# Performance work log

Hardware: AMD Instinct MI355X
Metric: run time of the kernel (lower is better)

## Reference

```python
import jax, jax.numpy as jnp
import numpy as np

B, D_IN, D_H = 8192, 512, 1024


def setup_inputs() -> dict:
    key = jax.random.key(0)
    ks = jax.random.split(key, 5)
    # Kaiming-normal-ish init: std = sqrt(2/fan_in)
    Wx = jax.random.normal(ks[0], (D_IN, 4 * D_H), jnp.float32) * np.sqrt(2.0 / D_IN)
    Wh = jax.random.normal(ks[1], (D_H, 4 * D_H), jnp.float32) * np.sqrt(2.0 / D_H)
    b = jnp.zeros((4 * D_H,), jnp.float32)
    x = jax.random.normal(ks[2], (B, D_IN), jnp.float32)
    h = jax.random.normal(ks[3], (B, D_H), jnp.float32)
    c = jax.random.normal(ks[4], (B, D_H), jnp.float32)
    return {"x": x, "h": h, "c": c, "Wx": Wx, "Wh": Wh, "b": b}


def reference(x, h, c, Wx, Wh, b):
    # Fused gate pre-activations: [B, 4H] in gate order (g, i, f, o)
    gates = x @ Wx + h @ Wh + b[None, :]
    g_in, i_in, f_in, o_in = jnp.split(gates, 4, axis=-1)
    g_out = jnp.tanh(g_in)
    i_out = jax.nn.sigmoid(i_in)
    # NOTE: faithful to the original source's bug — f_out and o_out both use i_in.
    f_out = jax.nn.sigmoid(i_in)
    o_out = jax.nn.sigmoid(i_in)
    c_new = g_out * i_out + f_out * c
    h_new = jnp.tanh(c_new) * o_out
    return h_new, c_new
```

## Files before the change

### kernel.cpp

```cpp
#include <hip/hip_runtime.h>
#include <hip/hip_bf16.h>
#include <cstdint>

#define BROWS 8192
#define DIN   512
#define DH    1024
#define KTOT  1536
#define NT    (KTOT / 64)

typedef __bf16 bf16x8 __attribute__((ext_vector_type(8)));
typedef __bf16 bf16x4 __attribute__((ext_vector_type(4)));
typedef float  f32x4  __attribute__((ext_vector_type(4)));

__device__ __forceinline__ void load16_to_lds(const void* gptr, void* lptr) {
    __builtin_amdgcn_global_load_lds(
        (const __attribute__((address_space(1))) uint32_t*)gptr,
        (__attribute__((address_space(3))) uint32_t*)lptr,
        16, 0, 0);
}

__global__ __launch_bounds__(256) void cvtA_kernel(
    const float* __restrict__ x, const float* __restrict__ h,
    __bf16* __restrict__ A) {
    int t = blockIdx.x * 256 + threadIdx.x;
    int row = t / 192;
    int j = t - row * 192;
    int kg = j * 8;
    const float* src = (kg < DIN) ? (x + (size_t)row * DIN + kg)
                                  : (h + (size_t)row * DH + (kg - DIN));
    float4 u = *(const float4*)src;
    float4 v = *(const float4*)(src + 4);
    bf16x8 o = { (__bf16)u.x, (__bf16)u.y, (__bf16)u.z, (__bf16)u.w,
                 (__bf16)v.x, (__bf16)v.y, (__bf16)v.z, (__bf16)v.w };
    int swz = (j * 16) ^ ((row & 7) << 4);
    *(bf16x8*)((char*)A + (size_t)row * 3072 + swz) = o;
}

__global__ __launch_bounds__(256) void cvtB_kernel(
    const float* __restrict__ Wx, const float* __restrict__ Wh,
    __bf16* __restrict__ Bt) {
    __shared__ float tile[32][33];
    int k0 = blockIdx.x * 32;
    int n0 = blockIdx.y * 32;
    int tx = threadIdx.x;
    int ty = threadIdx.y;
#pragma unroll
    for (int i = 0; i < 4; ++i) {
        int k = k0 + ty + 8 * i;
        float v = (k < DIN) ? Wx[(size_t)k * 4096 + n0 + tx]
                            : Wh[(size_t)(k - DIN) * 4096 + n0 + tx];
        tile[ty + 8 * i][tx] = v;
    }
    __syncthreads();
    int n = n0 + tx;
    int kk = ty * 4;
    bf16x4 o = { (__bf16)tile[kk][tx], (__bf16)tile[kk + 1][tx],
                 (__bf16)tile[kk + 2][tx], (__bf16)tile[kk + 3][tx] };
    int swz = ((k0 + kk) * 2) ^ ((n & 7) << 4);
    *(bf16x4*)((char*)Bt + (size_t)n * 3072 + swz) = o;
}


#define BARRIER  do { __builtin_amdgcn_sched_barrier(0); __builtin_amdgcn_s_barrier(); __builtin_amdgcn_sched_barrier(0); } while (0)
#define VMW(n)   do { asm volatile("s_waitcnt vmcnt(" #n ")" ::: "memory"); __builtin_amdgcn_sched_barrier(0); } while (0)
#define LGKM0    do { asm volatile("s_waitcnt lgkmcnt(0)" ::: "memory"); __builtin_amdgcn_sched_barrier(0); } while (0)

#define STAGE_A(buf, kt) do {                                                  \
    _Pragma("unroll")                                                          \
    for (int p_ = 0; p_ < 4; ++p_) {                                           \
        int row_ = p_ * 32 + r0;                                               \
        load16_to_lds(Ab + (size_t)(brow + row_) * 3072 + (kt) * 128 + cb,     \
                      sAb + (buf) * 32768 + row_ * 128 + cb);                  \
    }                                                                          \
    __builtin_amdgcn_sched_barrier(0);                                         \
} while (0)

#define STAGE_BG(buf, kt) do {                                                 \
    _Pragma("unroll")                                                          \
    for (int p_ = 0; p_ < 2; ++p_) {                                           \
        int row_ = p_ * 32 + r0;                                               \
        load16_to_lds(Bb + (size_t)(bnp + row_) * 3072 + (kt) * 128 + cb,      \
                      sAb + (buf) * 32768 + 16384 + row_ * 128 + cb);          \
    }                                                                          \
    __builtin_amdgcn_sched_barrier(0);                                         \
} while (0)

#define STAGE_BI(buf, kt) do {                                                 \
    _Pragma("unroll")                                                          \
    for (int p_ = 0; p_ < 2; ++p_) {                                           \
        int row_ = p_ * 32 + r0;                                               \
        load16_to_lds(Bb + (size_t)(1024 + bnp + row_) * 3072                  \
                          + (kt) * 128 + cb,                                   \
                      sAb + (buf) * 32768 + 16384 + (64 + row_) * 128 + cb);   \
    }                                                                          \
    __builtin_amdgcn_sched_barrier(0);                                         \
} while (0)

#define READ_A(c)                                                              \
    _Pragma("unroll")                                                          \
    for (int m_ = 0; m_ < 4; ++m_) {                                           \
        _Pragma("unroll")                                                      \
        for (int ks_ = 0; ks_ < 2; ++ks_) {                                    \
            aF[m_][ks_] = *(const bf16x8*)(sAb + (c) * 32768                   \
                + (wrow + m_ * 16 + l15) * 128                                 \
                + ((ks_ * 64 + l4x16) ^ swzkey));                              \
        }                                                                      \
    }

#define READ_BG(c)                                                             \
    _Pragma("unroll")                                                          \
    for (int n_ = 0; n_ < 2; ++n_) {                                           \
        _Pragma("unroll")                                                      \
        for (int ks_ = 0; ks_ < 2; ++ks_) {                                    \
            bgF[n_][ks_] = *(const bf16x8*)(sAb + (c) * 32768 + 16384          \
                + (wcol + n_ * 16 + l15) * 128                                 \
                + ((ks_ * 64 + l4x16) ^ swzkey));                              \
        }                                                                      \
    }

#define READ_BI(c)                                                             \
    _Pragma("unroll")                                                          \
    for (int n_ = 0; n_ < 2; ++n_) {                                           \
        _Pragma("unroll")                                                      \
        for (int ks_ = 0; ks_ < 2; ++ks_) {                                    \
            biF[n_][ks_] = *(const bf16x8*)(sAb + (c) * 32768 + 16384          \
                + (64 + wcol + n_ * 16 + l15) * 128                            \
                + ((ks_ * 64 + l4x16) ^ swzkey));                              \
        }                                                                      \
    }

#define MMA(ACC, BF) do {                                                      \
    __builtin_amdgcn_s_setprio(1);                                             \
    _Pragma("unroll")                                                          \
    for (int ks_ = 0; ks_ < 2; ++ks_) {                                        \
        _Pragma("unroll")                                                      \
        for (int m_ = 0; m_ < 4; ++m_) {                                       \
            _Pragma("unroll")                                                  \
            for (int n_ = 0; n_ < 2; ++n_) {                                   \
                ACC[m_][n_] = __builtin_amdgcn_mfma_f32_16x16x32_bf16(         \
                    aF[m_][ks_], BF[n_][ks_], ACC[m_][n_], 0, 0, 0);           \
            }                                                                  \
        }                                                                      \
    }                                                                          \
    __builtin_amdgcn_s_setprio(0);                                             \
    __builtin_amdgcn_sched_barrier(0);                                         \
} while (0)

__global__ __launch_bounds__(256, 2) void lstm_gemm_kernel(
    const __bf16* __restrict__ A,
    const __bf16* __restrict__ Bt,
    const float* __restrict__ bias,
    const float* __restrict__ c_in,
    float* __restrict__ out_h,
    float* __restrict__ out_c) {
    __shared__ char smem[65536];

    const int tid  = threadIdx.x;
    const int lane = tid & 63;
    const int wid  = tid >> 6;
    const int wr   = wid & 1;
    const int wc   = wid >> 1;

    const int bid   = blockIdx.x;
    const int q     = bid >> 3;
    const int band  = (bid & 7) * 8 + (q & 7);
    const int panel = q >> 3;
    const int brow  = band * 128;
    const int bnp   = panel * 64;

    const int l15    = lane & 15;
    const int l4x16  = (lane >> 4) * 16;
    const int swzkey = (l15 & 7) << 4;
    const int wrow   = wr * 64;
    const int wcol   = wc * 32;

    const int r0 = tid >> 3;
    const int cb = (tid & 7) * 16;

    const char* Ab = (const char*)A;
    const char* Bb = (const char*)Bt;
    char* sAb = smem;

    f32x4 accg[4][2], acci[4][2];
#pragma unroll
    for (int mi = 0; mi < 4; ++mi)
#pragma unroll
        for (int ni = 0; ni < 2; ++ni) {
            accg[mi][ni] = (f32x4){0.f, 0.f, 0.f, 0.f};
            acci[mi][ni] = (f32x4){0.f, 0.f, 0.f, 0.f};
        }

    bf16x8 aF[4][2], bgF[2][2], biF[2][2];

    STAGE_A(0, 0);
    STAGE_BG(0, 0);
    STAGE_BI(0, 0);

    for (int t = 0; t < NT - 1; ++t) {
        const int c  = t & 1;
        const int nb = c ^ 1;
        VMW(2); BARRIER;
        READ_A(c);
        READ_BG(c);
        STAGE_A(nb, t + 1);
        LGKM0;
        MMA(accg, bgF);
        VMW(4); BARRIER;
        READ_BI(c);
        STAGE_BG(nb, t + 1);
        STAGE_BI(nb, t + 1);
        LGKM0;
        MMA(acci, biF);
    }
    {
        const int c = (NT - 1) & 1;
        VMW(0); BARRIER;
        READ_A(c);
        READ_BG(c);
        READ_BI(c);
        LGKM0;
        MMA(accg, bgF);
        MMA(acci, biF);
    }

    const int R0 = brow + wrow;
    const int C0 = bnp + wcol;
    const int l4 = lane >> 4;
#pragma unroll
    for (int ni = 0; ni < 2; ++ni) {
        const int col = C0 + ni * 16 + l15;
        const float bg = bias[col];
        const float bi = bias[1024 + col];
#pragma unroll
        for (int mi = 0; mi < 4; ++mi) {
#pragma unroll
            for (int r = 0; r < 4; ++r) {
                const int row = R0 + mi * 16 + l4 * 4 + r;
                const float g_in = accg[mi][ni][r] + bg;
                const float i_in = acci[mi][ni][r] + bi;
                const float s  = 1.0f / (1.0f + __expf(-i_in));
                const float tg = 2.0f / (1.0f + __expf(-2.0f * g_in)) - 1.0f;
                const float cv = c_in[(size_t)row * DH + col];
                const float cn = s * (tg + cv);
                const float hn = (2.0f / (1.0f + __expf(-2.0f * cn)) - 1.0f) * s;
                out_h[(size_t)row * DH + col] = hn;
                out_c[(size_t)row * DH + col] = cn;
            }
        }
    }
}

extern "C" void kernel_launch(void* const* d_in, const int* in_sizes, int n_in,
                              void* d_out, int out_size, void* d_ws, size_t ws_size,
                              hipStream_t stream) {
    const float* x  = (const float*)d_in[0];
    const float* h  = (const float*)d_in[1];
    const float* c  = (const float*)d_in[2];
    const float* Wx = (const float*)d_in[3];
    const float* Wh = (const float*)d_in[4];
    const float* b  = (const float*)d_in[5];

    __bf16* A  = (__bf16*)d_ws;
    __bf16* Bt = (__bf16*)((char*)d_ws + (size_t)BROWS * KTOT * 2);

    float* out_h = (float*)d_out;
    float* out_c = out_h + (size_t)BROWS * DH;

    cvtA_kernel<<<(BROWS * (KTOT / 8)) / 256, 256, 0, stream>>>(x, h, A);
    cvtB_kernel<<<dim3(KTOT / 32, 2048 / 32), dim3(32, 8), 0, stream>>>(Wx, Wh, Bt);
    lstm_gemm_kernel<<<1024, 256, 0, stream>>>(A, Bt, b, c, out_h, out_c);
}
```

Baseline: 84.13 us.

## Use 256-row tiles with 8 waves and triple-buffered LDS pipeline

Doubles the GEMM block tile to 256 rows with 512 threads (8 waves) and halves the grid to 512 blocks. LDS staging becomes a three-deep ring buffer of 48KB stages, with prefetch two tiles ahead, replacing double buffering. Each A fragment now feeds both gate MMAs in one phase. This cuts B traffic per output and hides global latency better, at the cost of 144KB LDS (one block per CU) and an extra barrier per iteration.

```diff
diff --git a/kernel.cpp b/kernel.cpp
--- a/kernel.cpp
+++ b/kernel.cpp
@@ -65,71 +65,45 @@
 #define VMW(n)   do { asm volatile("s_waitcnt vmcnt(" #n ")" ::: "memory"); __builtin_amdgcn_sched_barrier(0); } while (0)
 #define LGKM0    do { asm volatile("s_waitcnt lgkmcnt(0)" ::: "memory"); __builtin_amdgcn_sched_barrier(0); } while (0)
 
-#define STAGE_A(buf, kt) do {                                                  \
+#define STAGE(obuf, kt) do {                                                   \
     _Pragma("unroll")                                                          \
     for (int p_ = 0; p_ < 4; ++p_) {                                           \
-        int row_ = p_ * 32 + r0;                                               \
+        int row_ = p_ * 64 + r0;                                               \
         load16_to_lds(Ab + (size_t)(brow + row_) * 3072 + (kt) * 128 + cb,     \
-                      sAb + (buf) * 32768 + row_ * 128 + cb);                  \
-    }                                                                          \
+                      sAb + (obuf) + row_ * 128 + cb);                         \
+    }                                                                          \
+    load16_to_lds(Bb + (size_t)(bnp + r0) * 3072 + (kt) * 128 + cb,            \
+                  sAb + (obuf) + 32768 + r0 * 128 + cb);                       \
+    load16_to_lds(Bb + (size_t)(1024 + bnp + r0) * 3072 + (kt) * 128 + cb,     \
+                  sAb + (obuf) + 32768 + (64 + r0) * 128 + cb);                \
     __builtin_amdgcn_sched_barrier(0);                                         \
 } while (0)
 
-#define STAGE_BG(buf, kt) do {                                                 \
-    _Pragma("unroll")                                                          \
-    for (int p_ = 0; p_ < 2; ++p_) {                                           \
-        int row_ = p_ * 32 + r0;                                               \
-        load16_to_lds(Bb + (size_t)(bnp + row_) * 3072 + (kt) * 128 + cb,      \
-                      sAb + (buf) * 32768 + 16384 + row_ * 128 + cb);          \
-    }                                                                          \
-    __builtin_amdgcn_sched_barrier(0);                                         \
-} while (0)
-
-#define STAGE_BI(buf, kt) do {                                                 \
-    _Pragma("unroll")                                                          \
-    for (int p_ = 0; p_ < 2; ++p_) {                                           \
-        int row_ = p_ * 32 + r0;                                               \
-        load16_to_lds(Bb + (size_t)(1024 + bnp + row_) * 3072                  \
-                          + (kt) * 128 + cb,                                   \
-                      sAb + (buf) * 32768 + 16384 + (64 + row_) * 128 + cb);   \
-    }                                                                          \
-    __builtin_amdgcn_sched_barrier(0);                                         \
-} while (0)
-
-#define READ_A(c)                                                              \
+#define READS(obuf) do {                                                       \
     _Pragma("unroll")                                                          \
     for (int m_ = 0; m_ < 4; ++m_) {                                           \
         _Pragma("unroll")                                                      \
         for (int ks_ = 0; ks_ < 2; ++ks_) {                                    \
-            aF[m_][ks_] = *(const bf16x8*)(sAb + (c) * 32768                   \
+            aF[m_][ks_] = *(const bf16x8*)(sAb + (obuf)                        \
                 + (wrow + m_ * 16 + l15) * 128                                 \
                 + ((ks_ * 64 + l4x16) ^ swzkey));                              \
         }                                                                      \
-    }
-
-#define READ_BG(c)                                                             \
+    }                                                                          \
     _Pragma("unroll")                                                          \
     for (int n_ = 0; n_ < 2; ++n_) {                                           \
         _Pragma("unroll")                                                      \
         for (int ks_ = 0; ks_ < 2; ++ks_) {                                    \
-            bgF[n_][ks_] = *(const bf16x8*)(sAb + (c) * 32768 + 16384          \
+            bgF[n_][ks_] = *(const bf16x8*)(sAb + (obuf) + 32768               \
                 + (wcol + n_ * 16 + l15) * 128                                 \
                 + ((ks_ * 64 + l4x16) ^ swzkey));                              \
-        }                                                                      \
-    }
-
-#define READ_BI(c)                                                             \
-    _Pragma("unroll")                                                          \
-    for (int n_ = 0; n_ < 2; ++n_) {                                           \
-        _Pragma("unroll")                                                      \
-        for (int ks_ = 0; ks_ < 2; ++ks_) {                                    \
-            biF[n_][ks_] = *(const bf16x8*)(sAb + (c) * 32768 + 16384          \
+            biF[n_][ks_] = *(const bf16x8*)(sAb + (obuf) + 32768               \
                 + (64 + wcol + n_ * 16 + l15) * 128                            \
                 + ((ks_ * 64 + l4x16) ^ swzkey));                              \
         }                                                                      \
-    }
-
-#define MMA(ACC, BF) do {                                                      \
+    }                                                                          \
+} while (0)
+
+#define MMA_ALL() do {                                                         \
     __builtin_amdgcn_s_setprio(1);                                             \
     _Pragma("unroll")                                                          \
     for (int ks_ = 0; ks_ < 2; ++ks_) {                                        \
@@ -137,8 +111,10 @@
         for (int m_ = 0; m_ < 4; ++m_) {                                       \
             _Pragma("unroll")                                                  \
             for (int n_ = 0; n_ < 2; ++n_) {                                   \
-                ACC[m_][n_] = __builtin_amdgcn_mfma_f32_16x16x32_bf16(         \
-                    aF[m_][ks_], BF[n_][ks_], ACC[m_][n_], 0, 0, 0);           \
+                accg[m_][n_] = __builtin_amdgcn_mfma_f32_16x16x32_bf16(        \
+                    aF[m_][ks_], bgF[n_][ks_], accg[m_][n_], 0, 0, 0);         \
+                acci[m_][n_] = __builtin_amdgcn_mfma_f32_16x16x32_bf16(        \
+                    aF[m_][ks_], biF[n_][ks_], acci[m_][n_], 0, 0, 0);         \
             }                                                                  \
         }                                                                      \
     }                                                                          \
@@ -146,26 +122,25 @@
     __builtin_amdgcn_sched_barrier(0);                                         \
 } while (0)
 
-__global__ __launch_bounds__(256, 2) void lstm_gemm_kernel(
+__global__ __launch_bounds__(512) void lstm_gemm_kernel(
     const __bf16* __restrict__ A,
     const __bf16* __restrict__ Bt,
     const float* __restrict__ bias,
     const float* __restrict__ c_in,
     float* __restrict__ out_h,
     float* __restrict__ out_c) {
-    __shared__ char smem[65536];
+    __shared__ char smem[147456];
 
     const int tid  = threadIdx.x;
     const int lane = tid & 63;
     const int wid  = tid >> 6;
-    const int wr   = wid & 1;
-    const int wc   = wid >> 1;
+    const int wr   = wid & 3;
+    const int wc   = wid >> 2;
 
     const int bid   = blockIdx.x;
-    const int q     = bid >> 3;
-    const int band  = (bid & 7) * 8 + (q & 7);
-    const int panel = q >> 3;
-    const int brow  = band * 128;
+    const int band  = (bid & 7) * 4 + ((bid >> 3) & 3);
+    const int panel = bid >> 5;
+    const int brow  = band * 256;
     const int bnp   = panel * 64;
 
     const int l15    = lane & 15;
@@ -192,35 +167,32 @@
 
     bf16x8 aF[4][2], bgF[2][2], biF[2][2];
 
-    STAGE_A(0, 0);
-    STAGE_BG(0, 0);
-    STAGE_BI(0, 0);
-
-    for (int t = 0; t < NT - 1; ++t) {
-        const int c  = t & 1;
-        const int nb = c ^ 1;
-        VMW(2); BARRIER;
-        READ_A(c);
-        READ_BG(c);
-        STAGE_A(nb, t + 1);
+    STAGE(0, 0);
+    STAGE(49152, 1);
+
+    int o0 = 0, o1 = 49152, o2 = 98304;
+    for (int t = 0; t < NT - 2; ++t) {
+        STAGE(o2, t + 2);
+        VMW(12);
+        BARRIER;
+        READS(o0);
         LGKM0;
-        MMA(accg, bgF);
-        VMW(4); BARRIER;
-        READ_BI(c);
-        STAGE_BG(nb, t + 1);
-        STAGE_BI(nb, t + 1);
+        BARRIER;
+        MMA_ALL();
+        int tmp = o0; o0 = o1; o1 = o2; o2 = tmp;
+    }
+    {
+        VMW(6); BARRIER;
+        READS(o0);
+        LGKM0; BARRIER;
+        MMA_ALL();
+        int tmp = o0; o0 = o1; o1 = o2; o2 = tmp;
+    }
+    {
+        VMW(0); BARRIER;
+        READS(o0);
         LGKM0;
-        MMA(acci, biF);
-    }
-    {
-        const int c = (NT - 1) & 1;
-        VMW(0); BARRIER;
-        READ_A(c);
-        READ_BG(c);
-        READ_BI(c);
-        LGKM0;
-        MMA(accg, bgF);
-        MMA(acci, biF);
+        MMA_ALL();
     }
 
     const int R0 = brow + wrow;
@@ -268,5 +240,5 @@
 
     cvtA_kernel<<<(BROWS * (KTOT / 8)) / 256, 256, 0, stream>>>(x, h, A);
     cvtB_kernel<<<dim3(KTOT / 32, 2048 / 32), dim3(32, 8), 0, stream>>>(Wx, Wh, Bt);
-    lstm_gemm_kernel<<<1024, 256, 0, stream>>>(A, Bt, b, c, out_h, out_c);
-}
+    lstm_gemm_kernel<<<512, 512, 0, stream>>>(A, Bt, b, c, out_h, out_c);
+}
```

Result: slower. 86.21 us (+2.5%).
